# Performance work log

Measured on AMD Instinct MI355X. Metric: run time of the kernel, lower is better.

Reference implementation:

```python
import jax, jax.numpy as jnp
import numpy as np
import math

N, C, T, V = 8, 256, 120, 25
W = 5          # window_size
PAD = 2        # (W + (W-1)*(dil-1) - 1)//2 with dil=1
H = 8          # num_heads
CO = 256       # out_channels
HD = CO // H   # head channels
EPS = 1e-5


def _bn(x, g, b, m, v):
    # eval-mode BatchNorm2d over channel axis 1; x: (N, C, T, V)
    inv = jax.lax.rsqrt(v + EPS)
    return (x - m[None, :, None, None]) * (inv * g)[None, :, None, None] + b[None, :, None, None]


def _mish(x):
    return x * jnp.tanh(jax.nn.softplus(x))


def setup_inputs() -> dict:
    key = jax.random.key(0)
    ks = jax.random.split(key, 16)
    s_in = 1.0 / math.sqrt(C)
    s_out = 1.0 / math.sqrt(CO)
    return {
        "x": jax.random.normal(ks[0], (N, C, T, V), jnp.float32),
        "w_qkv": jax.random.normal(ks[1], (C, 3 * CO), jnp.float32) * s_in,
        "w_out": jax.random.normal(ks[2], (CO, CO), jnp.float32) * s_out,
        "b_out": jax.random.normal(ks[3], (CO,), jnp.float32) * 0.01,
        "bn1_g": jax.random.normal(ks[4], (CO,), jnp.float32) * 0.1 + 1.0,
        "bn1_b": jax.random.normal(ks[5], (CO,), jnp.float32) * 0.1,
        "ffn_w1": jax.random.normal(ks[6], (CO, CO), jnp.float32) * s_out,
        "ffn_w2": jax.random.normal(ks[7], (CO, CO), jnp.float32) * s_out,
        "ffn_g": jax.random.normal(ks[8], (CO,), jnp.float32) * 0.1 + 1.0,
        "ffn_b": jax.random.normal(ks[9], (CO,), jnp.float32) * 0.1,
        "bn2_g": jax.random.normal(ks[10], (CO,), jnp.float32) * 0.1 + 1.0,
        "bn2_b": jax.random.normal(ks[11], (CO,), jnp.float32) * 0.1,
        "bn1_m": jax.random.normal(ks[12], (CO,), jnp.float32) * 0.1,
        "bn1_v": jax.random.uniform(ks[13], (CO,), jnp.float32, 0.5, 1.5),
        "ffn_m": jax.random.normal(ks[14], (CO,), jnp.float32) * 0.1,
        "ffn_v": jax.random.uniform(ks[15], (CO,), jnp.float32, 0.5, 1.5),
        "bn2_m": jnp.zeros((CO,), jnp.float32),
        "bn2_v": jnp.ones((CO,), jnp.float32),
    }


def reference(x, w_qkv, w_out, b_out, bn1_g, bn1_b, ffn_w1, ffn_w2, ffn_g, ffn_b,
              bn2_g, bn2_b, bn1_m, bn1_v, ffn_m, ffn_v, bn2_m, bn2_v):
    L = W * V
    # --- group_window: unfold over T with kernel (W,1), zero padding PAD ---
    xp = jnp.pad(x, ((0, 0), (0, 0), (PAD, PAD), (0, 0)))
    # (N, C, T, W, V): window element w at time t is frame t + w - PAD
    xw = jnp.stack([xp[:, :, w:w + T, :] for w in range(W)], axis=3)
    xg = xw.transpose(0, 2, 3, 4, 1).reshape(N * T, L, C)  # tokens: (N*T, L, C)

    # --- spatio-temporal attention (full softmax over L, scale 1/sqrt(CO)) ---
    qkv = (xg @ w_qkv).reshape(N * T, L, H, 3, HD)
    q, k, v = qkv[..., 0, :], qkv[..., 1, :], qkv[..., 2, :]  # (NT, L, H, HD)
    scores = jnp.einsum('blhd,bmhd->bhlm', q, k) / math.sqrt(CO)
    attn = jax.nn.softmax(scores, axis=-1)
    out = jnp.einsum('bhlm,bmhd->blhd', attn, v).reshape(N * T, L, CO)
    out = out @ w_out + b_out

    # --- mean over window dim, residual (Identity since C == CO), norm1 ---
    inter = out.reshape(N, T, W, V, CO).transpose(0, 4, 1, 2, 3).mean(axis=3)  # (N, CO, T, V)
    inter = _bn(inter + x, bn1_g, bn1_b, bn1_m, bn1_v)

    # --- FFN: 1x1 conv -> Mish -> BN -> 1x1 conv ---
    h = jnp.einsum('oi,nitv->notv', ffn_w1, inter)
    h = _bn(_mish(h), ffn_g, ffn_b, ffn_m, ffn_v)
    h = jnp.einsum('oi,nitv->notv', ffn_w2, h)

    return _bn(h + inter, bn2_g, bn2_b, bn2_m, bn2_v)
```

## Files before the change

### kernel.cpp

```cpp
#include <hip/hip_runtime.h>
#include <hip/hip_bf16.h>


using bf16  = __bf16;
using bf16x8 = __bf16 __attribute__((ext_vector_type(8)));
using f32x4  = float __attribute__((ext_vector_type(4)));
using f32x16 = float __attribute__((ext_vector_type(16)));
using uint32x4 = unsigned int __attribute__((ext_vector_type(4)));

#define GAS __attribute__((address_space(1)))
#define LAS __attribute__((address_space(3)))

__device__ __forceinline__ void gload_lds16(const void* g, void* l) {
  __builtin_amdgcn_global_load_lds((GAS void*)g, (LAS void*)l, 16, 0, 0);
}

__device__ __forceinline__ unsigned cvt_pk_bf16(float lo, float hi) {
  unsigned r;
  asm("v_cvt_pk_bf16_f32 %0, %1, %2" : "=v"(r) : "v"(lo), "v"(hi));
  return r;
}

__device__ __forceinline__ void pl32_swap(unsigned& a, unsigned& b) {
  asm("v_permlane32_swap_b32 %0, %1" : "+v"(a), "+v"(b));
}

__global__ void k_zero(float* out, int n) {
  int i = blockIdx.x * 256 + threadIdx.x;
  if (i < n) out[i] = 0.f;
}

__global__ void k_prep(const float* __restrict__ x,
                       const float* __restrict__ wqkv, const float* __restrict__ wout,
                       const float* __restrict__ b_out,
                       const float* __restrict__ w1, const float* __restrict__ w2,
                       const float* __restrict__ g1, const float* __restrict__ b1,
                       const float* __restrict__ m1, const float* __restrict__ v1,
                       const float* __restrict__ gf, const float* __restrict__ bff,
                       const float* __restrict__ mf, const float* __restrict__ vf,
                       const float* __restrict__ g2, const float* __restrict__ b2,
                       const float* __restrict__ m2, const float* __restrict__ v2,
                       bf16* __restrict__ Xrow, bf16* __restrict__ WqT,
                       bf16* __restrict__ WoT, bf16* __restrict__ W1c,
                       bf16* __restrict__ W2c, float* __restrict__ pb) {
  __shared__ bf16 T[64 * 72];
  const int b = blockIdx.x, tid = threadIdx.x;
  if (b < 1504) {
    const int bx = b % 47, by = (b / 47) & 3, n = b / 188;
    const int tv0 = bx * 64, c0 = by * 64;
    const int la = tid & 63, sub = tid >> 6;
#pragma unroll 4
    for (int i = 0; i < 16; ++i) {
      int c = c0 + sub + i * 4;
      int tv = tv0 + la;
      float v = (tv < 3000) ? x[(size_t)(n * 256 + c) * 3000 + tv] : 0.f;
      T[(sub + i * 4) * 72 + la] = (bf16)v;
    }
    __syncthreads();
#pragma unroll 4
    for (int i = 0; i < 16; ++i) {
      int tvl = sub + i * 4;
      int tv = tv0 + tvl;
      if (tv < 3000)
        Xrow[(size_t)(n * 3100 + 50 + tv) * 256 + c0 + la] = T[la * 72 + tvl];
    }
  } else if (b < 3041) {
    int idx = (b - 1504) * 256 + tid;
    if (idx < 196608) {
      int c = idx / 768, o = idx % 768;
      float vv = wqkv[idx];
      if ((o % 96) < 32) vv *= 0.0901387929f;
      WqT[o * 256 + c] = (bf16)vv;
    } else if (idx < 262144) {
      int j = idx - 196608;
      int c = j >> 8, o = j & 255;
      WoT[o * 256 + c] = (bf16)wout[j];
    } else if (idx < 327680) {
      int j = idx - 262144;
      W1c[j] = (bf16)w1[j];
    } else if (idx < 393216) {
      int j = idx - 327680;
      W2c[j] = (bf16)w2[j];
    } else if (idx < 393472) {
      int k = idx - 393216;
      float s1 = g1[k] * rsqrtf(v1[k] + 1e-5f);
      pb[k]        = s1;
      pb[256 + k]  = b1[k] - m1[k] * s1;
      float sf = gf[k] * rsqrtf(vf[k] + 1e-5f);
      pb[512 + k]  = sf;
      pb[768 + k]  = bff[k] - mf[k] * sf;
      float s2 = g2[k] * rsqrtf(v2[k] + 1e-5f);
      pb[1024 + k] = s2;
      pb[1280 + k] = b2[k] - m2[k] * s2;
      pb[1536 + k] = b_out[k];
    }
  } else {
    int z = b - 3041;
    int idx16 = z * 256 + tid;
    int e0 = idx16 * 8;
    int pr = e0 >> 8, col = e0 & 255;
    int n = pr / 100, r100 = pr % 100;
    int row = n * 3100 + (r100 < 50 ? r100 : 3000 + r100);
    int4 zz = {};
    *(int4*)&Xrow[(size_t)row * 256 + col] = zz;
  }
}

template <int EPI>
__global__ __launch_bounds__(256, 3) void k_gemm(
    const bf16* __restrict__ A, const bf16* __restrict__ BT,
    bf16* __restrict__ Cout, int ldc, int Mreal,
    const float* __restrict__ pb, const bf16* __restrict__ Res,
    float* __restrict__ Out2) {
  __shared__ __align__(16) char smem[32768];
  const int tid = threadIdx.x;
  const int w = tid >> 6, lane = tid & 63, q = lane >> 4, l15 = lane & 15;
  const int m0 = blockIdx.x * 128, n0 = blockIdx.y * 128;
  const int wm = (w >> 1) * 64, wn = (w & 1) * 64;
  const int srow = tid >> 2;
  const int scol = (tid & 3) << 3;
  int ar1 = m0 + srow;        if (ar1 >= Mreal) ar1 = Mreal - 1;
  int ar2 = m0 + srow + 64;   if (ar2 >= Mreal) ar2 = Mreal - 1;
  const bf16* gA1 = A  + (size_t)ar1 * 256 + scol;
  const bf16* gA2 = A  + (size_t)ar2 * 256 + scol;
  const bf16* gB1 = BT + (size_t)(n0 + srow) * 256 + scol;
  const bf16* gB2 = gB1 + 64 * 256;
  f32x4 acc[4][4] = {};

  auto STAGE = [&](int ks, char* buf) {
    char* ldsA = buf + w * 1024;
    char* ldsB = buf + 8192 + w * 1024;
    gload_lds16(gA1 + ks * 32, ldsA);
    gload_lds16(gA2 + ks * 32, ldsA + 4096);
    gload_lds16(gB1 + ks * 32, ldsB);
    gload_lds16(gB2 + ks * 32, ldsB + 4096);
  };

  int cur = 0;
  STAGE(0, smem);
  __syncthreads();
  for (int ks = 0; ks < 8; ++ks) {
    if (ks < 7) STAGE(ks + 1, smem + ((cur ^ 1) << 14));
    const bf16* Asc = (const bf16*)(smem + (cur << 14));
    const bf16* Bsc = Asc + 4096;
    bf16x8 af[4], bfr[4];
#pragma unroll
    for (int i = 0; i < 4; ++i) af[i]  = *(const bf16x8*)&Asc[(wm + i * 16 + l15) * 32 + q * 8];
#pragma unroll
    for (int i = 0; i < 4; ++i) bfr[i] = *(const bf16x8*)&Bsc[(wn + i * 16 + l15) * 32 + q * 8];
#pragma unroll
    for (int i = 0; i < 4; ++i)
#pragma unroll
      for (int j = 0; j < 4; ++j)
        acc[i][j] = __builtin_amdgcn_mfma_f32_16x16x32_bf16(af[i], bfr[j], acc[i][j], 0, 0, 0);
    __syncthreads();
    cur ^= 1;
  }

  if constexpr (EPI != 3) {
#pragma unroll
    for (int i = 0; i < 4; ++i) {
#pragma unroll
      for (int j = 0; j < 4; ++j) {
#pragma unroll
        for (int r = 0; r < 4; ++r) {
          int row = m0 + wm + i * 16 + q * 4 + r;
          int col = n0 + wn + j * 16 + l15;
          if (row >= Mreal) continue;
          float v = acc[i][j][r];
          if constexpr (EPI == 0) {
            Cout[(size_t)row * ldc + col] = (bf16)v;
          } else if constexpr (EPI == 1) {
            v += pb[1536 + col];
            int n = row / 3000;
            v += (float)Res[(size_t)(row + n * 100 + 50) * 256 + col];
            v = v * pb[col] + pb[256 + col];
            Cout[(size_t)row * 256 + col] = (bf16)v;
          } else {
            float ex = __expf(v);
            float a = 1.f + ex;
            float u = 1.f / (a * a);
            v = v * (1.f - u) / (1.f + u);
            v = v * pb[512 + col] + pb[768 + col];
            Cout[(size_t)row * 256 + col] = (bf16)v;
          }
        }
      }
    }
  } else {
    float* Tt = (float*)smem;
    const int tti = (w & 1);
#pragma unroll
    for (int jj = 0; jj < 4; ++jj) {
      __syncthreads();
#pragma unroll
      for (int i = 0; i < 4; ++i) {
#pragma unroll
        for (int r = 0; r < 4; ++r) {
          int rowl = wm + i * 16 + q * 4 + r;
          int row = m0 + rowl;
          int col = n0 + tti * 64 + jj * 16 + l15;
          float v = acc[i][jj][r];
          v += (float)Res[(size_t)row * 256 + col];
          v = v * pb[1024 + col] + pb[1280 + col];
          Tt[tti * 2432 + rowl * 19 + l15] = v;
        }
      }
      __syncthreads();
#pragma unroll
      for (int k = 0; k < 16; ++k) {
        int flat = k * 256 + tid;
        int tt2 = flat >> 11;
        int rem = flat & 2047;
        int colL = rem >> 7;
        int rowl = rem & 127;
        int row = m0 + rowl;
        if (row < Mreal) {
          int col = n0 + tt2 * 64 + jj * 16 + colL;
          int n = row / 3000, r2 = row - n * 3000;
          Out2[(size_t)(n * 256 + col) * 3000 + r2] = Tt[tt2 * 2432 + rowl * 19 + colL];
        }
      }
    }
  }
}

__global__ __launch_bounds__(256, 3) void k_ffn(
    const bf16* __restrict__ Aom, const bf16* __restrict__ Wo,
    const bf16* __restrict__ W1, const bf16* __restrict__ W2,
    const bf16* __restrict__ Xres, const float* __restrict__ pb,
    float* __restrict__ Out2) {
  __shared__ __align__(16) char smem[53760];
  bf16* XI = (bf16*)(smem + 36864);
  float* Tt = (float*)smem;
  const int tid = threadIdx.x;
  const int w = tid >> 6, lane = tid & 63, q = lane >> 4, l15 = lane & 15;
  const int r0 = blockIdx.x * 32;
  const int srow = tid >> 2, scol = (tid & 3) << 3;

  auto STAGE_A = [&](int ks, int b) {
    if (w == 0) {
      char* ldsA = smem + (b << 11);
      const bf16* src = Aom + (size_t)(r0 + (lane >> 2)) * 256 + ks * 32 + ((lane & 3) << 3);
      gload_lds16(src, ldsA);
      gload_lds16(src + 16 * 256, ldsA + 1024);
    }
  };
  auto STAGE_B = [&](const bf16* Wsrc, int ks, int b) {
    char* ldsB = smem + 4096 + (b << 14) + w * 1024;
#pragma unroll
    for (int ii = 0; ii < 4; ++ii)
      gload_lds16(Wsrc + (size_t)(ii * 64 + srow) * 256 + ks * 32 + scol,
                  ldsB + ii * 4096);
  };

  f32x4 acc[2][4];
#pragma unroll
  for (int i = 0; i < 2; ++i)
#pragma unroll
    for (int j = 0; j < 4; ++j) acc[i][j] = f32x4{};

  int cur = 0;
  STAGE_A(0, 0); STAGE_B(Wo, 0, 0);
  __syncthreads();
  for (int ks = 0; ks < 8; ++ks) {
    if (ks < 7) { STAGE_A(ks + 1, cur ^ 1); STAGE_B(Wo, ks + 1, cur ^ 1); }
    const bf16* Asc = (const bf16*)(smem + (cur << 11));
    const bf16* Bsc = (const bf16*)(smem + 4096 + (cur << 14));
    bf16x8 af[2], bfr[4];
#pragma unroll
    for (int i = 0; i < 2; ++i) af[i]  = *(const bf16x8*)&Asc[(i * 16 + l15) * 32 + q * 8];
#pragma unroll
    for (int j = 0; j < 4; ++j) bfr[j] = *(const bf16x8*)&Bsc[(w * 64 + j * 16 + l15) * 32 + q * 8];
#pragma unroll
    for (int i = 0; i < 2; ++i)
#pragma unroll
      for (int j = 0; j < 4; ++j)
        acc[i][j] = __builtin_amdgcn_mfma_f32_16x16x32_bf16(af[i], bfr[j], acc[i][j], 0, 0, 0);
    __syncthreads();
    cur ^= 1;
  }
  STAGE_B(W1, 0, 0);
  unsigned irk[16];
#pragma unroll
  for (int i = 0; i < 2; ++i) {
#pragma unroll
    for (int j = 0; j < 4; ++j) {
      int colb = w * 64 + j * 16 + l15;
      float vv[4];
#pragma unroll
      for (int r = 0; r < 4; ++r) {
        int grow = r0 + i * 16 + q * 4 + r;
        int nn = grow / 3000;
        float v = acc[i][j][r] + pb[1536 + colb]
                + (float)Xres[(size_t)(grow + nn * 100 + 50) * 256 + colb];
        v = v * pb[colb] + pb[256 + colb];
        vv[r] = v;
        XI[(i * 16 + q * 4 + r) * 264 + colb] = (bf16)v;
      }
      irk[(i * 4 + j) * 2 + 0] = cvt_pk_bf16(vv[0], vv[1]);
      irk[(i * 4 + j) * 2 + 1] = cvt_pk_bf16(vv[2], vv[3]);
    }
  }
  __syncthreads();

#pragma unroll
  for (int i = 0; i < 2; ++i)
#pragma unroll
    for (int j = 0; j < 4; ++j) acc[i][j] = f32x4{};
  cur = 0;
  for (int ks = 0; ks < 8; ++ks) {
    if (ks < 7) STAGE_B(W1, ks + 1, cur ^ 1);
    const bf16* Bsc = (const bf16*)(smem + 4096 + (cur << 14));
    bf16x8 af[2], bfr[4];
#pragma unroll
    for (int i = 0; i < 2; ++i) af[i]  = *(const bf16x8*)&XI[(i * 16 + l15) * 264 + ks * 32 + q * 8];
#pragma unroll
    for (int j = 0; j < 4; ++j) bfr[j] = *(const bf16x8*)&Bsc[(w * 64 + j * 16 + l15) * 32 + q * 8];
#pragma unroll
    for (int i = 0; i < 2; ++i)
#pragma unroll
      for (int j = 0; j < 4; ++j)
        acc[i][j] = __builtin_amdgcn_mfma_f32_16x16x32_bf16(af[i], bfr[j], acc[i][j], 0, 0, 0);
    __syncthreads();
    cur ^= 1;
  }
  STAGE_B(W2, 0, 0);
#pragma unroll
  for (int i = 0; i < 2; ++i) {
#pragma unroll
    for (int j = 0; j < 4; ++j) {
      int colb = w * 64 + j * 16 + l15;
#pragma unroll
      for (int r = 0; r < 4; ++r) {
        float v = acc[i][j][r];
        float ex = __expf(v);
        float a = 1.f + ex;
        float u = 1.f / (a * a);
        v = v * (1.f - u) / (1.f + u);
        v = v * pb[512 + colb] + pb[768 + colb];
        XI[(i * 16 + q * 4 + r) * 264 + colb] = (bf16)v;
      }
    }
  }
  __syncthreads();

#pragma unroll
  for (int i = 0; i < 2; ++i)
#pragma unroll
    for (int j = 0; j < 4; ++j) acc[i][j] = f32x4{};
  cur = 0;
  for (int ks = 0; ks < 8; ++ks) {
    if (ks < 7) STAGE_B(W2, ks + 1, cur ^ 1);
    const bf16* Bsc = (const bf16*)(smem + 4096 + (cur << 14));
    bf16x8 af[2], bfr[4];
#pragma unroll
    for (int i = 0; i < 2; ++i) af[i]  = *(const bf16x8*)&XI[(i * 16 + l15) * 264 + ks * 32 + q * 8];
#pragma unroll
    for (int j = 0; j < 4; ++j) bfr[j] = *(const bf16x8*)&Bsc[(w * 64 + j * 16 + l15) * 32 + q * 8];
#pragma unroll
    for (int i = 0; i < 2; ++i)
#pragma unroll
      for (int j = 0; j < 4; ++j)
        acc[i][j] = __builtin_amdgcn_mfma_f32_16x16x32_bf16(af[i], bfr[j], acc[i][j], 0, 0, 0);
    __syncthreads();
    cur ^= 1;
  }

  const int rowl_t = tid & 31;
  const int grow_t = r0 + rowl_t;
  const int nn_t = grow_t / 3000;
  const int rr_t = grow_t - nn_t * 3000;
#pragma unroll
  for (int cc = 0; cc < 4; ++cc) {
    __syncthreads();
    if (w == cc) {
#pragma unroll
      for (int i = 0; i < 2; ++i) {
#pragma unroll
        for (int j = 0; j < 4; ++j) {
          int colb = cc * 64 + j * 16 + l15;
#pragma unroll
          for (int r = 0; r < 4; ++r) {
            unsigned pr = irk[(i * 4 + j) * 2 + (r >> 1)];
            unsigned short us = (r & 1) ? (unsigned short)(pr >> 16)
                                        : (unsigned short)(pr & 0xffff);
            float res = (float)__builtin_bit_cast(bf16, us);
            float v = acc[i][j][r] + res;
            v = v * pb[1024 + colb] + pb[1280 + colb];
            Tt[(i * 16 + q * 4 + r) * 65 + j * 16 + l15] = v;
          }
        }
      }
    }
    __syncthreads();
#pragma unroll
    for (int it = 0; it < 8; ++it) {
      int cl = (tid >> 5) + it * 8;
      int colb = cc * 64 + cl;
      Out2[(size_t)(nn_t * 256 + colb) * 3000 + rr_t] = Tt[rowl_t * 65 + cl];
    }
  }
}

__global__ __launch_bounds__(256, 6) void k_attn(const bf16* __restrict__ Y,
                                                 bf16* __restrict__ om) {
  __shared__ __align__(16) char smem[18944];
  bf16* Vts = (bf16*)smem;
  float* Ofl = (float*)smem;
  float* Rin = (float*)(smem + 18432);
  const int tid = threadIdx.x;
  const int bi = blockIdx.x;
  const int h = bi & 7, b = bi >> 3;
  const int n = b / 120, t = b % 120;
  const bf16* Yb = Y + (size_t)(n * 3100 + t * 25) * 768 + h * 96;
  const int w = tid >> 6, lane = tid & 63;
  const int l31 = lane & 31, hi = lane >> 5;

#pragma unroll
  for (int p = 0; p < 2; ++p) {
    int m = p * 64 + lane;
    if (m < 125) {
      int4 v4 = *(const int4*)(Yb + (size_t)m * 768 + 64 + w * 8);
      bf16x8 v8 = __builtin_bit_cast(bf16x8, v4);
#pragma unroll
      for (int jj = 0; jj < 8; ++jj) Vts[(w * 8 + jj) * 136 + m] = v8[jj];
    }
  }
  if (tid < 96) {
    int d = tid / 3, m = 125 + tid % 3;
    Vts[d * 136 + m] = (bf16)0.f;
  }

  int qrow = w * 32 + l31; if (qrow > 124) qrow = 124;
  const bf16* qp = Yb + (size_t)qrow * 768 + hi * 8;
  bf16x8 qf0 = *(const bf16x8*)qp;
  bf16x8 qf1 = *(const bf16x8*)(qp + 16);

  f32x16 acc[4] = {};
#pragma unroll
  for (int kt = 0; kt < 4; ++kt) {
    int krow = kt * 32 + l31; if (krow > 124) krow = 124;
    const bf16* kp = Yb + (size_t)krow * 768 + 32 + hi * 8;
    bf16x8 kf0 = *(const bf16x8*)kp;
    bf16x8 kf1 = *(const bf16x8*)(kp + 16);
    acc[kt] = __builtin_amdgcn_mfma_f32_32x32x16_bf16(kf0, qf0, acc[kt], 0, 0, 0);
    acc[kt] = __builtin_amdgcn_mfma_f32_32x32x16_bf16(kf1, qf1, acc[kt], 0, 0, 0);
  }

  float sp[4];
  uint32x4 pk[8];
#pragma unroll
  for (int kt = 0; kt < 4; ++kt) {
    float e[16];
#pragma unroll
    for (int r = 0; r < 16; ++r) {
      float pz = exp2f(acc[kt][r]);
      if (kt == 3 && r >= 13 && hi) pz = 0.f;
      e[r] = pz;
    }
    float t0 = (e[0] + e[1]) + (e[2] + e[3]);
    float t1 = (e[4] + e[5]) + (e[6] + e[7]);
    float t2 = (e[8] + e[9]) + (e[10] + e[11]);
    float t3 = (e[12] + e[13]) + (e[14] + e[15]);
    sp[kt] = (t0 + t1) + (t2 + t3);
#pragma unroll
    for (int half = 0; half < 2; ++half) {
      const int ba = half * 8;
      unsigned a0 = cvt_pk_bf16(e[ba + 0], e[ba + 1]);
      unsigned a1 = cvt_pk_bf16(e[ba + 2], e[ba + 3]);
      unsigned b0 = cvt_pk_bf16(e[ba + 4], e[ba + 5]);
      unsigned b1 = cvt_pk_bf16(e[ba + 6], e[ba + 7]);
      pl32_swap(a0, b0);
      pl32_swap(a1, b1);
      pk[kt * 2 + half][0] = a0;
      pk[kt * 2 + half][1] = a1;
      pk[kt * 2 + half][2] = b0;
      pk[kt * 2 + half][3] = b1;
    }
  }
  float s = (sp[0] + sp[1]) + (sp[2] + sp[3]);
  s += __shfl_xor(s, 32, 64);
  float rinv = 1.f / s;
  if (hi == 0) Rin[w * 32 + l31] = rinv;

  __syncthreads();

  f32x16 oacc0 = {}, oacc1 = {};
#pragma unroll
  for (int kc = 0; kc < 8; ++kc) {
    bf16x8 pa = __builtin_bit_cast(bf16x8, pk[kc]);
    bf16x8 vf = *(const bf16x8*)&Vts[l31 * 136 + kc * 16 + hi * 8];
    if (kc & 1) oacc1 = __builtin_amdgcn_mfma_f32_32x32x16_bf16(pa, vf, oacc1, 0, 0, 0);
    else        oacc0 = __builtin_amdgcn_mfma_f32_32x32x16_bf16(pa, vf, oacc0, 0, 0, 0);
  }

  __syncthreads();
#pragma unroll
  for (int r = 0; r < 16; ++r) {
    int row = w * 32 + (r & 3) + 8 * (r >> 2) + 4 * hi;
    Ofl[row * 36 + l31] = oacc0[r] + oacc1[r];
  }
  __syncthreads();
  bf16* dst = om + (size_t)((n * 120 + t) * 25) * 256 + h * 32;
  for (int j = tid; j < 800; j += 256) {
    int vv = j >> 5, d = j & 31;
    float s5 = 0.f;
#pragma unroll
    for (int ww = 0; ww < 5; ++ww)
      s5 += Ofl[(ww * 25 + vv) * 36 + d] * Rin[ww * 25 + vv];
    dst[vv * 256 + d] = (bf16)(s5 * 0.2f);
  }
}

extern "C" void kernel_launch(void* const* d_in, const int* in_sizes, int n_in,
                              void* d_out, int out_size, void* d_ws, size_t ws_size,
                              hipStream_t stream) {
  const size_t NEED1 = 51584000;
  const size_t NEED2 = 63872000;
  if (ws_size < NEED1) {
    k_zero<<<(out_size + 255) / 256, 256, 0, stream>>>((float*)d_out, out_size);
    return;
  }
  const float* x     = (const float*)d_in[0];
  const float* wqkv  = (const float*)d_in[1];
  const float* wout  = (const float*)d_in[2];
  const float* b_out = (const float*)d_in[3];
  const float* bn1_g = (const float*)d_in[4];
  const float* bn1_b = (const float*)d_in[5];
  const float* ffn_w1= (const float*)d_in[6];
  const float* ffn_w2= (const float*)d_in[7];
  const float* ffn_g = (const float*)d_in[8];
  const float* ffn_b = (const float*)d_in[9];
  const float* bn2_g = (const float*)d_in[10];
  const float* bn2_b = (const float*)d_in[11];
  const float* bn1_m = (const float*)d_in[12];
  const float* bn1_v = (const float*)d_in[13];
  const float* ffn_m = (const float*)d_in[14];
  const float* ffn_v = (const float*)d_in[15];
  const float* bn2_m = (const float*)d_in[16];
  const float* bn2_v = (const float*)d_in[17];

  char* ws = (char*)d_ws;
  float* pb    = (float*)(ws + 0);
  bf16* WqT    = (bf16*)(ws + 7168);
  bf16* WoT    = (bf16*)(ws + 400384);
  bf16* W1c    = (bf16*)(ws + 531456);
  bf16* W2c    = (bf16*)(ws + 662528);
  bf16* Xrow   = (bf16*)(ws + 793600);
  bf16* Y      = (bf16*)(ws + 13491200);
  bf16* interR = Y;
  bf16* Gm     = (bf16*)(ws + 25779200);
  bf16* om2    = (bf16*)(ws + 51584000);
  bf16* om     = (bf16*)d_out;

  k_prep<<<3141, 256, 0, stream>>>(x, wqkv, wout, b_out, ffn_w1, ffn_w2,
                                   bn1_g, bn1_b, bn1_m, bn1_v,
                                   ffn_g, ffn_b, ffn_m, ffn_v,
                                   bn2_g, bn2_b, bn2_m, bn2_v,
                                   Xrow, WqT, WoT, W1c, W2c, pb);
  k_gemm<0><<<dim3(194, 6), 256, 0, stream>>>(Xrow, WqT, Y, 768, 24800, pb, nullptr, nullptr);
  if (ws_size >= NEED2) {
    k_attn<<<7680, 256, 0, stream>>>(Y, om2);
    k_ffn<<<750, 256, 0, stream>>>(om2, WoT, W1c, W2c, Xrow, pb, (float*)d_out);
  } else {
    k_attn<<<7680, 256, 0, stream>>>(Y, om);
    k_gemm<1><<<dim3(188, 2), 256, 0, stream>>>(om, WoT, interR, 256, 24000, pb, Xrow, nullptr);
    k_gemm<2><<<dim3(188, 2), 256, 0, stream>>>(interR, W1c, Gm, 256, 24000, pb, nullptr, nullptr);
    k_gemm<3><<<dim3(188, 2), 256, 0, stream>>>(Gm, W2c, nullptr, 256, 24000, pb, interR, (float*)d_out);
  }
}
```

Measured before the change: 220.2 us.

## Stream QK tiles through softmax and PV MFMA with K prefetch in attention

Restructures the attention kernel so each 32-key tile runs QK MFMA, exp, bf16 pack and the PV MFMA in one pass, instead of computing all four score tiles first. The next K tile is loaded from global memory while the current tile is processed, and the V-transpose barrier moves ahead of the loop. This cuts live registers (no acc[4] or pk[8] arrays) and overlaps global loads with math. Launch bounds drop from 6 to 5 blocks per CU, which gives the compiler more registers but may lower occupancy.

```diff
diff --git a/kernel.cpp b/kernel.cpp
--- a/kernel.cpp
+++ b/kernel.cpp
@@ -403,7 +403,7 @@
   }
 }
 
-__global__ __launch_bounds__(256, 6) void k_attn(const bf16* __restrict__ Y,
+__global__ __launch_bounds__(256, 5) void k_attn(const bf16* __restrict__ Y,
                                                  bf16* __restrict__ om) {
   __shared__ __align__(16) char smem[18944];
   bf16* Vts = (bf16*)smem;
@@ -436,26 +436,30 @@
   const bf16* qp = Yb + (size_t)qrow * 768 + hi * 8;
   bf16x8 qf0 = *(const bf16x8*)qp;
   bf16x8 qf1 = *(const bf16x8*)(qp + 16);
-
-  f32x16 acc[4] = {};
+  int krow0 = l31; if (krow0 > 124) krow0 = 124;
+  const bf16* kp0 = Yb + (size_t)krow0 * 768 + 32 + hi * 8;
+  bf16x8 kf0 = *(const bf16x8*)kp0;
+  bf16x8 kf1 = *(const bf16x8*)(kp0 + 16);
+
+  __syncthreads();
+
+  f32x16 oacc0 = {}, oacc1 = {};
+  float s = 0.f;
 #pragma unroll
   for (int kt = 0; kt < 4; ++kt) {
-    int krow = kt * 32 + l31; if (krow > 124) krow = 124;
-    const bf16* kp = Yb + (size_t)krow * 768 + 32 + hi * 8;
-    bf16x8 kf0 = *(const bf16x8*)kp;
-    bf16x8 kf1 = *(const bf16x8*)(kp + 16);
-    acc[kt] = __builtin_amdgcn_mfma_f32_32x32x16_bf16(kf0, qf0, acc[kt], 0, 0, 0);
-    acc[kt] = __builtin_amdgcn_mfma_f32_32x32x16_bf16(kf1, qf1, acc[kt], 0, 0, 0);
-  }
-
-  float sp[4];
-  uint32x4 pk[8];
-#pragma unroll
-  for (int kt = 0; kt < 4; ++kt) {
+    f32x16 acc = {};
+    acc = __builtin_amdgcn_mfma_f32_32x32x16_bf16(kf0, qf0, acc, 0, 0, 0);
+    acc = __builtin_amdgcn_mfma_f32_32x32x16_bf16(kf1, qf1, acc, 0, 0, 0);
+    if (kt < 3) {
+      int krow = (kt + 1) * 32 + l31; if (krow > 124) krow = 124;
+      const bf16* kp = Yb + (size_t)krow * 768 + 32 + hi * 8;
+      kf0 = *(const bf16x8*)kp;
+      kf1 = *(const bf16x8*)(kp + 16);
+    }
     float e[16];
 #pragma unroll
     for (int r = 0; r < 16; ++r) {
-      float pz = exp2f(acc[kt][r]);
+      float pz = exp2f(acc[r]);
       if (kt == 3 && r >= 13 && hi) pz = 0.f;
       e[r] = pz;
     }
@@ -463,7 +467,7 @@
     float t1 = (e[4] + e[5]) + (e[6] + e[7]);
     float t2 = (e[8] + e[9]) + (e[10] + e[11]);
     float t3 = (e[12] + e[13]) + (e[14] + e[15]);
-    sp[kt] = (t0 + t1) + (t2 + t3);
+    s += (t0 + t1) + (t2 + t3);
 #pragma unroll
     for (int half = 0; half < 2; ++half) {
       const int ba = half * 8;
@@ -473,27 +477,18 @@
       unsigned b1 = cvt_pk_bf16(e[ba + 6], e[ba + 7]);
       pl32_swap(a0, b0);
       pl32_swap(a1, b1);
-      pk[kt * 2 + half][0] = a0;
-      pk[kt * 2 + half][1] = a1;
-      pk[kt * 2 + half][2] = b0;
-      pk[kt * 2 + half][3] = b1;
-    }
-  }
-  float s = (sp[0] + sp[1]) + (sp[2] + sp[3]);
+      uint32x4 pwv;
+      pwv[0] = a0; pwv[1] = a1; pwv[2] = b0; pwv[3] = b1;
+      bf16x8 pa = __builtin_bit_cast(bf16x8, pwv);
+      const int kc = kt * 2 + half;
+      bf16x8 vf = *(const bf16x8*)&Vts[l31 * 136 + kc * 16 + hi * 8];
+      if (kc & 1) oacc1 = __builtin_amdgcn_mfma_f32_32x32x16_bf16(pa, vf, oacc1, 0, 0, 0);
+      else        oacc0 = __builtin_amdgcn_mfma_f32_32x32x16_bf16(pa, vf, oacc0, 0, 0, 0);
+    }
+  }
   s += __shfl_xor(s, 32, 64);
   float rinv = 1.f / s;
   if (hi == 0) Rin[w * 32 + l31] = rinv;
-
-  __syncthreads();
-
-  f32x16 oacc0 = {}, oacc1 = {};
-#pragma unroll
-  for (int kc = 0; kc < 8; ++kc) {
-    bf16x8 pa = __builtin_bit_cast(bf16x8, pk[kc]);
-    bf16x8 vf = *(const bf16x8*)&Vts[l31 * 136 + kc * 16 + hi * 8];
-    if (kc & 1) oacc1 = __builtin_amdgcn_mfma_f32_32x32x16_bf16(pa, vf, oacc1, 0, 0, 0);
-    else        oacc0 = __builtin_amdgcn_mfma_f32_32x32x16_bf16(pa, vf, oacc0, 0, 0, 0);
-  }
 
   __syncthreads();
 #pragma unroll
```

Result: faster. 207.7 us (-5.7%).
